# Performance work log

Measured on AMD Instinct MI355X. Metric: run time of the kernel, lower is better.

The kernel has to match this reference:

```python
import jax, jax.numpy as jnp
import numpy as np

B, D_IN, N_CLASSES, N_NODES, D_2D = 512, 512, 16, 100000, 2
EPS = 1e-8  # torch cosine_similarity eps


def setup_inputs() -> dict:
    key = jax.random.key(0)
    k0, k1, k2, k3, k4 = jax.random.split(key, 5)
    logits = jax.random.normal(k0, (B, N_CLASSES), dtype=jnp.float32)
    train_data = jax.random.normal(k1, (B, D_IN), dtype=jnp.float32)
    all_nodes = jax.random.normal(k2, (N_NODES, N_CLASSES), dtype=jnp.float32)
    all_nodes_2d = jax.random.normal(k3, (N_NODES, D_2D), dtype=jnp.float32)
    W = jax.random.normal(k4, (D_IN, D_2D), dtype=jnp.float32) * 0.02
    b = jnp.zeros((D_2D,), dtype=jnp.float32)
    return {"logits": logits, "train_data": train_data, "all_nodes": all_nodes,
            "all_nodes_2d": all_nodes_2d, "W": W, "b": b}


def reference(logits, train_data, all_nodes, all_nodes_2d, W, b):
    # model(train_data): linear 512 -> 2 projection
    emb = train_data @ W + b                                  # (B, 2)
    probs = jax.nn.softmax(logits, axis=1)                    # (B, C)
    pred_class = jnp.argmax(probs, axis=1)                    # (B,)
    node_class = jnp.argmax(all_nodes, axis=1)                # (N,)

    # cosine similarity between each sample's probs and every node (B, N)
    p_norm = jnp.linalg.norm(probs, axis=1, keepdims=True)    # (B, 1)
    n_norm = jnp.linalg.norm(all_nodes, axis=1)               # (N,)
    sim = (probs @ all_nodes.T) / jnp.maximum(p_norm * n_norm[None, :], EPS)

    # masked nearest-neighbor search: only nodes whose argmax class matches
    # the sample's predicted class are candidates (equivalent to the per-sample
    # boolean filtering + argmax in the original loop; first-match tie-break).
    masked_sim = jnp.where(pred_class[:, None] == node_class[None, :], sim, -jnp.inf)
    closest = jnp.argmax(masked_sim, axis=1)                  # (B,)

    target = all_nodes_2d[closest]                            # (B, 2)
    per_sample_mse = jnp.mean((emb - target) ** 2, axis=1)    # (B,)
    return jnp.mean(per_sample_mse)                           # scalar
```

## Files before the change

kernel.cpp:

```cpp
#include <hip/hip_runtime.h>

#define BATCH 512
#define DIN 512
#define NCLS 16
#define NNODES 100000
#define CBLK 256
#define NODE_BLOCKS ((NNODES + CBLK - 1) / CBLK)

#define WS_BEST   0
#define WS_PROBS  4096
#define WS_EMB    36864
#define WS_SORT   40960
#define WS_OFF    43008
#define WS_DONE   43136

__device__ __forceinline__ unsigned ford(float f) {
    unsigned bits = __float_as_uint(f);
    return (bits & 0x80000000u) ? ~bits : (bits | 0x80000000u);
}

__global__ __launch_bounds__(512) void prep_kernel(
    const float* __restrict__ logits,
    const float* __restrict__ train_data,
    const float* __restrict__ W,
    const float* __restrict__ bvec,
    float* __restrict__ probs,
    float* __restrict__ emb,
    int* __restrict__ sorted_ids,
    int* __restrict__ class_off,
    unsigned long long* __restrict__ best,
    unsigned int* __restrict__ done) {
    if (blockIdx.x < 64) {
        const int wave = threadIdx.x >> 6;
        const int lane = threadIdx.x & 63;
        const int s = blockIdx.x * 8 + wave;
        const float* td = train_data + s * DIN;
        const float2* W2 = (const float2*)W;
        float a0 = 0.f, a1 = 0.f;
        for (int k = lane; k < DIN; k += 64) {
            float t = td[k];
            float2 w = W2[k];
            a0 += t * w.x;
            a1 += t * w.y;
        }
        for (int off = 32; off; off >>= 1) {
            a0 += __shfl_down(a0, off);
            a1 += __shfl_down(a1, off);
        }
        if (lane == 0) {
            emb[2 * s]     = a0 + bvec[0];
            emb[2 * s + 1] = a1 + bvec[1];
        }
    } else {
        __shared__ int scnt[NCLS];
        __shared__ int soff[NCLS + 1];
        const int s = threadIdx.x;
        if (s < NCLS) scnt[s] = 0;

        const float4* lg = (const float4*)(logits + s * NCLS);
        float4 x0 = lg[0], x1 = lg[1], x2 = lg[2], x3 = lg[3];
        float v[NCLS] = {x0.x, x0.y, x0.z, x0.w, x1.x, x1.y, x1.z, x1.w,
                         x2.x, x2.y, x2.z, x2.w, x3.x, x3.y, x3.z, x3.w};
        float m = v[0];
        int pred = 0;
        #pragma unroll
        for (int j = 1; j < NCLS; ++j)
            if (v[j] > m) { m = v[j]; pred = j; }
        float sum = 0.f;
        #pragma unroll
        for (int j = 0; j < NCLS; ++j) { v[j] = expf(v[j] - m); sum += v[j]; }
        float inv = 1.0f / sum;
        float4* p4 = (float4*)(probs + s * NCLS);
        p4[0] = make_float4(v[0] * inv, v[1] * inv, v[2] * inv, v[3] * inv);
        p4[1] = make_float4(v[4] * inv, v[5] * inv, v[6] * inv, v[7] * inv);
        p4[2] = make_float4(v[8] * inv, v[9] * inv, v[10] * inv, v[11] * inv);
        p4[3] = make_float4(v[12] * inv, v[13] * inv, v[14] * inv, v[15] * inv);

        best[s] = 0ull;

        __syncthreads();
        int pos = atomicAdd(&scnt[pred], 1);
        __syncthreads();
        if (s == 0) {
            int acc = 0;
            for (int c = 0; c < NCLS; ++c) { soff[c] = acc; acc += scnt[c]; }
            soff[NCLS] = acc;
            *done = 0u;
        }
        __syncthreads();
        sorted_ids[soff[pred] + pos] = s;
        if (s <= NCLS) class_off[s] = soff[s];
    }
}

__global__ __launch_bounds__(256) void nodes_kernel(
    const float* __restrict__ all_nodes,
    const float* __restrict__ probs,
    const int* __restrict__ sorted_ids,
    const int* __restrict__ class_off,
    unsigned long long* __restrict__ best,
    unsigned int* __restrict__ done,
    const float* __restrict__ emb,
    const float* __restrict__ all_nodes_2d,
    float* __restrict__ out) {
    __shared__ float4 sp4[4 * BATCH];
    __shared__ unsigned long long lbest[BATCH];
    __shared__ int ssort[BATCH];
    __shared__ int soff[NCLS + 1];
    __shared__ int slast;
    __shared__ float part[4];

    const int t = threadIdx.x;

    const float4* p4 = (const float4*)probs;
    for (int i = t; i < 4 * BATCH; i += CBLK)
        sp4[(i & 3) * BATCH + (i >> 2)] = p4[i];
    for (int i = t; i < BATCH; i += CBLK) {
        lbest[i] = 0ull;
        ssort[i] = sorted_ids[i];
    }
    if (t <= NCLS) soff[t] = class_off[t];
    __syncthreads();

    const int n = blockIdx.x * CBLK + t;
    if (n < NNODES) {
        const float4* nv = (const float4*)(all_nodes + n * NCLS);
        float4 v0 = nv[0], v1 = nv[1], v2 = nv[2], v3 = nv[3];
        float vals[NCLS] = {v0.x, v0.y, v0.z, v0.w, v1.x, v1.y, v1.z, v1.w,
                            v2.x, v2.y, v2.z, v2.w, v3.x, v3.y, v3.z, v3.w};
        int cls = 0;
        float m = vals[0];
        float nrm2 = 0.f;
        #pragma unroll
        for (int j = 0; j < NCLS; ++j) {
            if (j > 0 && vals[j] > m) { m = vals[j]; cls = j; }
            nrm2 += vals[j] * vals[j];
        }
        float inv_norm = 1.0f / sqrtf(nrm2);
        unsigned low = 0xFFFFFFFFu - (unsigned)n;

        const int i0 = soff[cls], i1 = soff[cls + 1];
        for (int i = i0; i < i1; ++i) {
            int s = ssort[i];
            float4 a0 = sp4[s];
            float4 a1 = sp4[BATCH + s];
            float4 a2 = sp4[2 * BATCH + s];
            float4 a3 = sp4[3 * BATCH + s];
            float dot = a0.x * v0.x + a0.y * v0.y + a0.z * v0.z + a0.w * v0.w
                      + a1.x * v1.x + a1.y * v1.y + a1.z * v1.z + a1.w * v1.w
                      + a2.x * v2.x + a2.y * v2.y + a2.z * v2.z + a2.w * v2.w
                      + a3.x * v3.x + a3.y * v3.y + a3.z * v3.z + a3.w * v3.w;
            float sim = dot * inv_norm;
            unsigned long long packed =
                ((unsigned long long)ford(sim) << 32) | (unsigned long long)low;
            if (packed > lbest[s]) atomicMax(&lbest[s], packed);
        }
    }
    __syncthreads();
    for (int i = t; i < BATCH; i += CBLK) {
        unsigned long long b = lbest[i];
        if (b) atomicMax(&best[i], b);
    }
    __threadfence();
    __syncthreads();
    if (t == 0)
        slast = (atomicAdd(done, 1u) == (unsigned)(gridDim.x - 1)) ? 1 : 0;
    __syncthreads();
    if (slast) {
        float v = 0.f;
        for (int i = t; i < BATCH; i += CBLK) {
            unsigned long long p = atomicMax(&best[i], 0ull);
            int idx = (p == 0ull) ? 0
                                  : (int)(0xFFFFFFFFu - (unsigned)(p & 0xFFFFFFFFull));
            float2 tgt = ((const float2*)all_nodes_2d)[idx];
            float2 e = ((const float2*)emb)[i];
            float d0 = e.x - tgt.x;
            float d1 = e.y - tgt.y;
            v += 0.5f * (d0 * d0 + d1 * d1);
        }
        for (int off = 32; off; off >>= 1) v += __shfl_down(v, off);
        if ((t & 63) == 0) part[t >> 6] = v;
        __syncthreads();
        if (t == 0)
            out[0] = (part[0] + part[1] + part[2] + part[3]) / (float)BATCH;
    }
}

extern "C" void kernel_launch(void* const* d_in, const int* in_sizes, int n_in,
                              void* d_out, int out_size, void* d_ws, size_t ws_size,
                              hipStream_t stream) {
    const float* logits       = (const float*)d_in[0];
    const float* train_data   = (const float*)d_in[1];
    const float* all_nodes    = (const float*)d_in[2];
    const float* all_nodes_2d = (const float*)d_in[3];
    const float* W            = (const float*)d_in[4];
    const float* bvec         = (const float*)d_in[5];
    float* out = (float*)d_out;

    char* ws = (char*)d_ws;
    unsigned long long* best = (unsigned long long*)(ws + WS_BEST);
    float* probs             = (float*)(ws + WS_PROBS);
    float* emb               = (float*)(ws + WS_EMB);
    int* sorted_ids          = (int*)(ws + WS_SORT);
    int* class_off           = (int*)(ws + WS_OFF);
    unsigned int* done       = (unsigned int*)(ws + WS_DONE);

    prep_kernel<<<65, 512, 0, stream>>>(logits, train_data, W, bvec,
                                        probs, emb, sorted_ids, class_off,
                                        best, done);

    nodes_kernel<<<NODE_BLOCKS, CBLK, 0, stream>>>(all_nodes, probs,
                                                   sorted_ids, class_off,
                                                   best, done,
                                                   emb, all_nodes_2d, out);
}
```

Before: 107.4 us.

## Invert node search loop to per-sample threads with per-block bucketed nodes and separate merge

Each block now buckets its 256 nodes by argmax class into shared memory. Each thread then handles two samples and scans only the same-class nodes of that block, keeping its running best in a register instead of issuing shared 64-bit atomicMax. Per-block results go to a global array (391×512 entries), which a new merge kernel reduces per sample before computing the MSE. This removes the sorting and atomic traffic but adds a third launch and roughly 1.6 MB of intermediate writes and reads.

```diff
diff --git a/kernel.cpp b/kernel.cpp
--- a/kernel.cpp
+++ b/kernel.cpp
@@ -7,12 +7,12 @@
 #define CBLK 256
 #define NODE_BLOCKS ((NNODES + CBLK - 1) / CBLK)
 
-#define WS_BEST   0
-#define WS_PROBS  4096
-#define WS_EMB    36864
-#define WS_SORT   40960
-#define WS_OFF    43008
-#define WS_DONE   43136
+#define WS_VAL   0
+#define WS_PROBS 1601536
+#define WS_EMB   1634304
+#define WS_PCLS  1638400
+#define WS_MSE   1640448
+#define WS_DONE  1642496
 
 __device__ __forceinline__ unsigned ford(float f) {
     unsigned bits = __float_as_uint(f);
@@ -26,9 +26,7 @@
     const float* __restrict__ bvec,
     float* __restrict__ probs,
     float* __restrict__ emb,
-    int* __restrict__ sorted_ids,
-    int* __restrict__ class_off,
-    unsigned long long* __restrict__ best,
+    int* __restrict__ pcls,
     unsigned int* __restrict__ done) {
     if (blockIdx.x < 64) {
         const int wave = threadIdx.x >> 6;
@@ -52,11 +50,7 @@
             emb[2 * s + 1] = a1 + bvec[1];
         }
     } else {
-        __shared__ int scnt[NCLS];
-        __shared__ int soff[NCLS + 1];
         const int s = threadIdx.x;
-        if (s < NCLS) scnt[s] = 0;
-
         const float4* lg = (const float4*)(logits + s * NCLS);
         float4 x0 = lg[0], x1 = lg[1], x2 = lg[2], x3 = lg[3];
         float v[NCLS] = {x0.x, x0.y, x0.z, x0.w, x1.x, x1.y, x1.z, x1.w,
@@ -75,56 +69,28 @@
         p4[1] = make_float4(v[4] * inv, v[5] * inv, v[6] * inv, v[7] * inv);
         p4[2] = make_float4(v[8] * inv, v[9] * inv, v[10] * inv, v[11] * inv);
         p4[3] = make_float4(v[12] * inv, v[13] * inv, v[14] * inv, v[15] * inv);
-
-        best[s] = 0ull;
-
-        __syncthreads();
-        int pos = atomicAdd(&scnt[pred], 1);
-        __syncthreads();
-        if (s == 0) {
-            int acc = 0;
-            for (int c = 0; c < NCLS; ++c) { soff[c] = acc; acc += scnt[c]; }
-            soff[NCLS] = acc;
-            *done = 0u;
-        }
-        __syncthreads();
-        sorted_ids[soff[pred] + pos] = s;
-        if (s <= NCLS) class_off[s] = soff[s];
+        pcls[s] = pred;
+        if (s == 0) *done = 0u;
     }
 }
 
 __global__ __launch_bounds__(256) void nodes_kernel(
     const float* __restrict__ all_nodes,
     const float* __restrict__ probs,
-    const int* __restrict__ sorted_ids,
-    const int* __restrict__ class_off,
-    unsigned long long* __restrict__ best,
-    unsigned int* __restrict__ done,
-    const float* __restrict__ emb,
-    const float* __restrict__ all_nodes_2d,
-    float* __restrict__ out) {
-    __shared__ float4 sp4[4 * BATCH];
-    __shared__ unsigned long long lbest[BATCH];
-    __shared__ int ssort[BATCH];
-    __shared__ int soff[NCLS + 1];
-    __shared__ int slast;
-    __shared__ float part[4];
+    const int* __restrict__ pcls,
+    unsigned long long* __restrict__ val) {
+    __shared__ float4 snode[4 * CBLK];
+    __shared__ float sinv[CBLK];
+    __shared__ unsigned short clist[NCLS * CBLK];
+    __shared__ int scnt[NCLS];
 
     const int t = threadIdx.x;
-
-    const float4* p4 = (const float4*)probs;
-    for (int i = t; i < 4 * BATCH; i += CBLK)
-        sp4[(i & 3) * BATCH + (i >> 2)] = p4[i];
-    for (int i = t; i < BATCH; i += CBLK) {
-        lbest[i] = 0ull;
-        ssort[i] = sorted_ids[i];
-    }
-    if (t <= NCLS) soff[t] = class_off[t];
+    if (t < NCLS) scnt[t] = 0;
     __syncthreads();
 
-    const int n = blockIdx.x * CBLK + t;
-    if (n < NNODES) {
-        const float4* nv = (const float4*)(all_nodes + n * NCLS);
+    const int nid = blockIdx.x * CBLK + t;
+    if (nid < NNODES) {
+        const float4* nv = (const float4*)(all_nodes + nid * NCLS);
         float4 v0 = nv[0], v1 = nv[1], v2 = nv[2], v3 = nv[3];
         float vals[NCLS] = {v0.x, v0.y, v0.z, v0.w, v1.x, v1.y, v1.z, v1.w,
                             v2.x, v2.y, v2.z, v2.w, v3.x, v3.y, v3.z, v3.w};
@@ -136,53 +102,84 @@
             if (j > 0 && vals[j] > m) { m = vals[j]; cls = j; }
             nrm2 += vals[j] * vals[j];
         }
-        float inv_norm = 1.0f / sqrtf(nrm2);
-        unsigned low = 0xFFFFFFFFu - (unsigned)n;
-
-        const int i0 = soff[cls], i1 = soff[cls + 1];
-        for (int i = i0; i < i1; ++i) {
-            int s = ssort[i];
-            float4 a0 = sp4[s];
-            float4 a1 = sp4[BATCH + s];
-            float4 a2 = sp4[2 * BATCH + s];
-            float4 a3 = sp4[3 * BATCH + s];
+        snode[t]            = v0;
+        snode[CBLK + t]     = v1;
+        snode[2 * CBLK + t] = v2;
+        snode[3 * CBLK + t] = v3;
+        sinv[t] = 1.0f / sqrtf(nrm2);
+        int pos = atomicAdd(&scnt[cls], 1);
+        clist[cls * CBLK + pos] = (unsigned short)t;
+    }
+    __syncthreads();
+
+    const int base = blockIdx.x * CBLK;
+    #pragma unroll
+    for (int h = 0; h < 2; ++h) {
+        const int s = t + h * CBLK;
+        const float4* p4 = (const float4*)(probs + s * NCLS);
+        float4 a0 = p4[0], a1 = p4[1], a2 = p4[2], a3 = p4[3];
+        const int c = pcls[s];
+        const int cnt = scnt[c];
+        const unsigned short* lst = &clist[c * CBLK];
+        unsigned long long best = 0ull;
+        for (int i = 0; i < cnt; ++i) {
+            const int n = lst[i];
+            float4 v0 = snode[n];
+            float4 v1 = snode[CBLK + n];
+            float4 v2 = snode[2 * CBLK + n];
+            float4 v3 = snode[3 * CBLK + n];
             float dot = a0.x * v0.x + a0.y * v0.y + a0.z * v0.z + a0.w * v0.w
                       + a1.x * v1.x + a1.y * v1.y + a1.z * v1.z + a1.w * v1.w
                       + a2.x * v2.x + a2.y * v2.y + a2.z * v2.z + a2.w * v2.w
                       + a3.x * v3.x + a3.y * v3.y + a3.z * v3.z + a3.w * v3.w;
-            float sim = dot * inv_norm;
+            float sim = dot * sinv[n];
             unsigned long long packed =
-                ((unsigned long long)ford(sim) << 32) | (unsigned long long)low;
-            if (packed > lbest[s]) atomicMax(&lbest[s], packed);
-        }
-    }
-    __syncthreads();
-    for (int i = t; i < BATCH; i += CBLK) {
-        unsigned long long b = lbest[i];
-        if (b) atomicMax(&best[i], b);
+                ((unsigned long long)ford(sim) << 32)
+                | (unsigned long long)(0xFFFFFFFFu - (unsigned)(base + n));
+            best = (packed > best) ? packed : best;
+        }
+        val[blockIdx.x * BATCH + s] = best;
+    }
+}
+
+__global__ __launch_bounds__(64) void merge_kernel(
+    const unsigned long long* __restrict__ val,
+    const float* __restrict__ emb,
+    const float* __restrict__ all_nodes_2d,
+    float* __restrict__ mse,
+    unsigned int* __restrict__ done,
+    float* __restrict__ out) {
+    const int s = blockIdx.x;
+    const int k = threadIdx.x;
+
+    unsigned long long m = 0ull;
+    for (int b = k; b < NODE_BLOCKS; b += 64) {
+        unsigned long long v = val[b * BATCH + s];
+        m = (v > m) ? v : m;
+    }
+    for (int off = 32; off; off >>= 1) {
+        unsigned long long o = __shfl_down(m, off);
+        m = (o > m) ? o : m;
+    }
+    if (k == 0) {
+        int idx = (m == 0ull) ? 0
+                              : (int)(0xFFFFFFFFu - (unsigned)(m & 0xFFFFFFFFull));
+        float2 tg = ((const float2*)all_nodes_2d)[idx];
+        float2 e = ((const float2*)emb)[s];
+        float d0 = e.x - tg.x;
+        float d1 = e.y - tg.y;
+        mse[s] = 0.5f * (d0 * d0 + d1 * d1);
     }
     __threadfence();
-    __syncthreads();
-    if (t == 0)
-        slast = (atomicAdd(done, 1u) == (unsigned)(gridDim.x - 1)) ? 1 : 0;
-    __syncthreads();
-    if (slast) {
-        float v = 0.f;
-        for (int i = t; i < BATCH; i += CBLK) {
-            unsigned long long p = atomicMax(&best[i], 0ull);
-            int idx = (p == 0ull) ? 0
-                                  : (int)(0xFFFFFFFFu - (unsigned)(p & 0xFFFFFFFFull));
-            float2 tgt = ((const float2*)all_nodes_2d)[idx];
-            float2 e = ((const float2*)emb)[i];
-            float d0 = e.x - tgt.x;
-            float d1 = e.y - tgt.y;
-            v += 0.5f * (d0 * d0 + d1 * d1);
-        }
-        for (int off = 32; off; off >>= 1) v += __shfl_down(v, off);
-        if ((t & 63) == 0) part[t >> 6] = v;
-        __syncthreads();
-        if (t == 0)
-            out[0] = (part[0] + part[1] + part[2] + part[3]) / (float)BATCH;
+    unsigned ticket = 0u;
+    if (k == 0) ticket = atomicAdd(done, 1u);
+    ticket = __shfl(ticket, 0);
+    if (ticket == (unsigned)(gridDim.x - 1)) {
+        __threadfence();
+        float ssum = 0.f;
+        for (int i = k; i < BATCH; i += 64) ssum += mse[i];
+        for (int off = 32; off; off >>= 1) ssum += __shfl_down(ssum, off);
+        if (k == 0) out[0] = ssum / (float)BATCH;
     }
 }
 
@@ -198,19 +195,18 @@
     float* out = (float*)d_out;
 
     char* ws = (char*)d_ws;
-    unsigned long long* best = (unsigned long long*)(ws + WS_BEST);
-    float* probs             = (float*)(ws + WS_PROBS);
-    float* emb               = (float*)(ws + WS_EMB);
-    int* sorted_ids          = (int*)(ws + WS_SORT);
-    int* class_off           = (int*)(ws + WS_OFF);
-    unsigned int* done       = (unsigned int*)(ws + WS_DONE);
+    unsigned long long* val = (unsigned long long*)(ws + WS_VAL);
+    float* probs            = (float*)(ws + WS_PROBS);
+    float* emb              = (float*)(ws + WS_EMB);
+    int* pcls               = (int*)(ws + WS_PCLS);
+    float* mse              = (float*)(ws + WS_MSE);
+    unsigned int* done      = (unsigned int*)(ws + WS_DONE);
 
     prep_kernel<<<65, 512, 0, stream>>>(logits, train_data, W, bvec,
-                                        probs, emb, sorted_ids, class_off,
-                                        best, done);
-
-    nodes_kernel<<<NODE_BLOCKS, CBLK, 0, stream>>>(all_nodes, probs,
-                                                   sorted_ids, class_off,
-                                                   best, done,
-                                                   emb, all_nodes_2d, out);
-}
+                                        probs, emb, pcls, done);
+
+    nodes_kernel<<<NODE_BLOCKS, CBLK, 0, stream>>>(all_nodes, probs, pcls, val);
+
+    merge_kernel<<<BATCH, 64, 0, stream>>>(val, emb, all_nodes_2d,
+                                           mse, done, out);
+}
```

Result: no change. 107.9 us (+0.5%).
